# Performance work log

Measured on AMD Instinct MI355X. Metric: run time of the kernel, lower is better.

The kernel has to match this reference:

```python
import jax, jax.numpy as jnp
import numpy as np

N, INC, MID, K = 65536, 256, 64, 16
EPS = 1e-5  # BatchNorm1d default eps


def _bn(x, g, b, m, v):
    # eval-mode BatchNorm1d applied per-channel along the last dim
    return (x - m) * (g * jax.lax.rsqrt(v + EPS)) + b


def setup_inputs() -> dict:
    key = jax.random.key(0)
    ks = jax.random.split(key, 40)
    rn = lambda i, shape, s=0.05: (jax.random.normal(ks[i], shape, jnp.float32) * s)
    pv = lambda i, n: jax.random.uniform(ks[i], (n,), jnp.float32, 0.5, 1.5)  # positive running var
    return {
        "feats": jax.random.normal(ks[0], (N, INC), jnp.float32),
        "pos": jax.random.uniform(ks[1], (N, 3), jnp.float32) * 10.0,
        "idx": jax.random.randint(ks[2], (N, K), 0, N),
        "w_in": rn(3, (MID, INC)),
        "w_q": rn(4, (MID, MID)), "b_q": rn(5, (MID,)),
        "w_k": rn(6, (MID, MID)), "b_k": rn(7, (MID,)),
        "w_v": rn(8, (MID, MID)), "b_v": rn(9, (MID,)),
        # pos_enc: Linear(3,3) -> BN(3) -> ReLU -> Linear(3,mid) -> BN(mid) -> ReLU
        "pe_w1": rn(10, (3, 3)), "pe_b1": rn(11, (3,)),
        "pe_g1": jnp.ones(3), "pe_be1": rn(12, (3,)), "pe_m1": rn(13, (3,)), "pe_v1": pv(14, 3),
        "pe_w2": rn(15, (MID, 3)), "pe_b2": rn(16, (MID,)),
        "pe_g2": jnp.ones(MID), "pe_be2": rn(17, (MID,)), "pe_m2": rn(18, (MID,)), "pe_v2": pv(19, MID),
        # mlp_gamma: Linear(mid,mid) -> BN(mid) -> ReLU -> Linear(mid,mid) -> BN(mid) -> ReLU
        "ga_w1": rn(20, (MID, MID)), "ga_b1": rn(21, (MID,)),
        "ga_g1": jnp.ones(MID), "ga_be1": rn(22, (MID,)), "ga_m1": rn(23, (MID,)), "ga_v1": pv(24, MID),
        "ga_w2": rn(25, (MID, MID)), "ga_b2": rn(26, (MID,)),
        "ga_g2": jnp.ones(MID), "ga_be2": rn(27, (MID,)), "ga_m2": rn(28, (MID,)), "ga_v2": pv(29, MID),
        "w_out": rn(30, (INC, MID)),
    }


def reference(feats, pos, w_in, w_q, b_q, w_k, b_k, w_v, b_v,
              pe_w1, pe_b1, pe_g1, pe_be1, pe_m1, pe_v1,
              pe_w2, pe_b2, pe_g2, pe_be2, pe_m2, pe_v2,
              ga_w1, ga_b1, ga_g1, ga_be1, ga_m1, ga_v1,
              ga_w2, ga_b2, ga_g2, ga_be2, ga_m2, ga_v2,
              w_out, idx):
    xx = feats @ w_in.T                              # [N, mid]
    q = xx @ w_q.T + b_q
    k = xx @ w_k.T + b_k
    v = xx @ w_v.T + b_v
    xv = v[idx]                                      # [N, K, mid] gather
    xk = k[idx]                                      # [N, K, mid]
    xpos = pos[idx]                                  # [N, K, 3]
    # pos_enc
    p = jax.nn.relu(_bn(xpos @ pe_w1.T + pe_b1, pe_g1, pe_be1, pe_m1, pe_v1))
    p = jax.nn.relu(_bn(p @ pe_w2.T + pe_b2, pe_g2, pe_be2, pe_m2, pe_v2))  # [N, K, mid]
    # vector attention logits
    w = xk - q[:, None, :] + p                       # [N, K, mid]
    # mlp_gamma
    w = jax.nn.relu(_bn(w @ ga_w1.T + ga_b1, ga_g1, ga_be1, ga_m1, ga_v1))
    w = jax.nn.relu(_bn(w @ ga_w2.T + ga_b2, ga_g2, ga_be2, ga_m2, ga_v2))
    w = jax.nn.softmax(w, axis=1)                    # softmax over neighbors
    out = jnp.sum((xv + p) * w, axis=1)              # [N, mid]
    out = out @ w_out.T                              # [N, inc]
    return out + feats
```

## Files before the change

kernel.cpp:

```cpp
#include <hip/hip_runtime.h>

#define NPTS 65536
#define INC  256
#define MID  64
#define KNB  16
#define WSTR 72

#define WIN_S   0
#define WQ_S    16384
#define WK_S    20480
#define WV_S    24576
#define GA1_S   28672
#define GA2_S   32768
#define WOUT_S  36864
#define NFRAG_ENT 6656

typedef __attribute__((ext_vector_type(8))) short short8;
typedef __attribute__((ext_vector_type(4))) float f32x4;

#define MFMA(a, b, c) __builtin_amdgcn_mfma_f32_16x16x32_bf16((a), (b), (c), 0, 0, 0)
#define WBAR() __builtin_amdgcn_wave_barrier()

__device__ inline float bf2f(unsigned short s) {
    unsigned int u = ((unsigned int)s) << 16;
    return __builtin_bit_cast(float, u);
}
__device__ inline unsigned int pk_bf16(float lo, float hi) {
    unsigned int r;
    asm("v_cvt_pk_bf16_f32 %0, %1, %2" : "=v"(r) : "v"(lo), "v"(hi));
    return r;
}
__device__ inline short f2bf(float f) { return (short)pk_bf16(f, f); }

__device__ inline short8 cvtf8(f32x4 a, f32x4 b) {
    union { unsigned int u[4]; short8 s; } r;
    r.u[0] = pk_bf16(a[0], a[1]); r.u[1] = pk_bf16(a[2], a[3]);
    r.u[2] = pk_bf16(b[0], b[1]); r.u[3] = pk_bf16(b[2], b[3]);
    return r.s;
}
__device__ inline short8 load_cvt8(const float* __restrict__ p) {
    const f32x4* v = (const f32x4*)p;
    return cvtf8(v[0], v[1]);
}
__device__ inline short8 load_cvt8s(const float* __restrict__ p, float scale) {
    const f32x4* v = (const f32x4*)p;
    f32x4 a = v[0], b = v[1];
    #pragma unroll
    for (int i = 0; i < 4; i++) { a[i] *= scale; b[i] *= scale; }
    return cvtf8(a, b);
}

__global__ __launch_bounds__(256) void k_prep(
    const float* __restrict__ w_in, const float* __restrict__ w_q,
    const float* __restrict__ w_k, const float* __restrict__ w_v,
    const float* __restrict__ ga_w1, const float* __restrict__ ga_w2,
    const float* __restrict__ w_out,
    const float* __restrict__ ga_g1, const float* __restrict__ ga_v1,
    const float* __restrict__ ga_g2, const float* __restrict__ ga_v2,
    short* __restrict__ wbuf)
{
    int gid = blockIdx.x * 256 + threadIdx.x;
    if (gid >= NFRAG_ENT) return;
    if (gid < 2048) {
        int e = gid, f = e >> 6, ln = e & 63;
        int nt = f & 3, ks = f >> 2;
        int row = nt * 16 + (ln & 15), col = ks * 32 + (ln >> 4) * 8;
        *(short8*)&wbuf[(size_t)gid * 8] = load_cvt8(w_in + (size_t)row * INC + col);
    } else if (gid < 4608) {
        int seg = (gid - 2048) >> 9;
        int e = (gid - 2048) & 511;
        const float* m = seg == 0 ? w_q : seg == 1 ? w_k : seg == 2 ? w_v
                       : seg == 3 ? ga_w1 : ga_w2;
        int f = e >> 6, ln = e & 63;
        int nt = f & 3, ks = f >> 2;
        int row = nt * 16 + (ln & 15), col = ks * 32 + (ln >> 4) * 8;
        float scale = 1.f;
        if (seg == 3)      scale = ga_g1[row] * rsqrtf(ga_v1[row] + 1e-5f);
        else if (seg == 4) scale = ga_g2[row] * rsqrtf(ga_v2[row] + 1e-5f);
        *(short8*)&wbuf[(size_t)gid * 8] = load_cvt8s(m + (size_t)row * MID + col, scale);
    } else {
        int e = gid - 4608, f = e >> 6, ln = e & 63;
        int nt = f >> 1, ks = f & 1;
        int row = nt * 16 + (ln & 15), col = ks * 32 + (ln >> 4) * 8;
        *(short8*)&wbuf[(size_t)gid * 8] = load_cvt8(w_out + (size_t)row * MID + col);
    }
}

__global__ __launch_bounds__(256) void k_qkv(
    const float* __restrict__ feats, const short* __restrict__ wfrag,
    const float* __restrict__ pos,
    const float* __restrict__ b_q, const float* __restrict__ b_k,
    const float* __restrict__ b_v,
    const float* __restrict__ pe_w1, const float* __restrict__ pe_b1,
    const float* __restrict__ pe_g1, const float* __restrict__ pe_be1,
    const float* __restrict__ pe_m1, const float* __restrict__ pe_v1,
    const float* __restrict__ pe_w2, const float* __restrict__ pe_b2,
    const float* __restrict__ pe_g2, const float* __restrict__ pe_be2,
    const float* __restrict__ pe_m2, const float* __restrict__ pe_v2,
    const float* __restrict__ ga_b1, const float* __restrict__ ga_g1,
    const float* __restrict__ ga_be1, const float* __restrict__ ga_m1,
    const float* __restrict__ ga_v1,
    short* __restrict__ q1f_out, unsigned* __restrict__ kv_out)
{
    __shared__ __align__(16) short XL[4][16 * WSTR];
    __shared__ float PS[4][16 * 4];
    const int tid = threadIdx.x;
    const int wave = tid >> 6, lane = tid & 63;
    const int l15 = lane & 15, quad = lane >> 4;
    const int rb = (blockIdx.x * 4 + wave) * 16;

    if (lane < 16) {
        float s0 = pe_g1[0] * rsqrtf(pe_v1[0] + 1e-5f);
        float s1 = pe_g1[1] * rsqrtf(pe_v1[1] + 1e-5f);
        float sc = pe_g1[2] * rsqrtf(pe_v1[2] + 1e-5f);
        float px = pos[(size_t)(rb + lane) * 3 + 0];
        float py = pos[(size_t)(rb + lane) * 3 + 1];
        float pz = pos[(size_t)(rb + lane) * 3 + 2];
        PS[wave][lane * 4 + 0] =
            fmaxf((px * pe_w1[0] + py * pe_w1[1] + pz * pe_w1[2] + pe_b1[0] - pe_m1[0]) * s0 + pe_be1[0], 0.f);
        PS[wave][lane * 4 + 1] =
            fmaxf((px * pe_w1[3] + py * pe_w1[4] + pz * pe_w1[5] + pe_b1[1] - pe_m1[1]) * s1 + pe_be1[1], 0.f);
        PS[wave][lane * 4 + 2] =
            fmaxf((px * pe_w1[6] + py * pe_w1[7] + pz * pe_w1[8] + pe_b1[2] - pe_m1[2]) * sc + pe_be1[2], 0.f);
    }

    float w2c0[4], w2c1[4], w2c2[4], s2c[4], sh2c[4], bet1[4], bqc[4], bkc[4], bvc[4];
    #pragma unroll
    for (int nt = 0; nt < 4; nt++) {
        int ch = nt * 16 + l15;
        w2c0[nt] = pe_w2[ch * 3 + 0]; w2c1[nt] = pe_w2[ch * 3 + 1]; w2c2[nt] = pe_w2[ch * 3 + 2];
        float s2 = pe_g2[ch] * rsqrtf(pe_v2[ch] + 1e-5f);
        s2c[nt] = s2;
        sh2c[nt] = (pe_b2[ch] - pe_m2[ch]) * s2 + pe_be2[ch];
        float s1 = ga_g1[ch] * rsqrtf(ga_v1[ch] + 1e-5f);
        bet1[nt] = ga_b1[ch] * s1 + ga_be1[ch] - ga_m1[ch] * s1;
        bqc[nt] = b_q[ch]; bkc[nt] = b_k[ch]; bvc[nt] = b_v[ch];
    }

    f32x4 acc[4];
    #pragma unroll
    for (int nt = 0; nt < 4; nt++) acc[nt] = (f32x4){0.f, 0.f, 0.f, 0.f};
    const float* arow = feats + (size_t)(rb + l15) * INC + quad * 8;
    #pragma unroll
    for (int ks = 0; ks < 8; ks++) {
        short8 a = load_cvt8(arow + ks * 32);
        #pragma unroll
        for (int nt = 0; nt < 4; nt++) {
            short8 b = *(const short8*)&wfrag[WIN_S + (size_t)((ks * 4 + nt) * 64 + lane) * 8];
            acc[nt] = MFMA(a, b, acc[nt]);
        }
    }
    #pragma unroll
    for (int nt = 0; nt < 4; nt++) {
        unsigned int p01 = pk_bf16(acc[nt][0], acc[nt][1]);
        unsigned int p23 = pk_bf16(acc[nt][2], acc[nt][3]);
        XL[wave][(quad * 4 + 0) * WSTR + nt * 16 + l15] = (short)p01;
        XL[wave][(quad * 4 + 1) * WSTR + nt * 16 + l15] = (short)(p01 >> 16);
        XL[wave][(quad * 4 + 2) * WSTR + nt * 16 + l15] = (short)p23;
        XL[wave][(quad * 4 + 3) * WSTR + nt * 16 + l15] = (short)(p23 >> 16);
    }
    WBAR();
    short8 a0 = *(const short8*)&XL[wave][l15 * WSTR + quad * 8];
    short8 a1 = *(const short8*)&XL[wave][l15 * WSTR + 32 + quad * 8];
    WBAR();

    float p10[4], p11[4], p12[4];
    #pragma unroll
    for (int r = 0; r < 4; r++) {
        p10[r] = PS[wave][(quad * 4 + r) * 4 + 0];
        p11[r] = PS[wave][(quad * 4 + r) * 4 + 1];
        p12[r] = PS[wave][(quad * 4 + r) * 4 + 2];
    }
    float pe_[4][4];
    #pragma unroll
    for (int nt = 0; nt < 4; nt++)
        #pragma unroll
        for (int r = 0; r < 4; r++)
            pe_[nt][r] = fmaxf((p10[r] * w2c0[nt] + p11[r] * w2c1[nt] + p12[r] * w2c2[nt])
                               * s2c[nt] + sh2c[nt], 0.f);

    #pragma unroll
    for (int nt = 0; nt < 4; nt++) {
        short8 b0 = *(const short8*)&wfrag[WQ_S + (size_t)((nt) * 64 + lane) * 8];
        short8 b1 = *(const short8*)&wfrag[WQ_S + (size_t)((4 + nt) * 64 + lane) * 8];
        f32x4 c = (f32x4){0.f, 0.f, 0.f, 0.f};
        c = MFMA(a0, b0, c); c = MFMA(a1, b1, c);
        unsigned int p01 = pk_bf16(c[0] + bqc[nt], c[1] + bqc[nt]);
        unsigned int p23 = pk_bf16(c[2] + bqc[nt], c[3] + bqc[nt]);
        XL[wave][(quad * 4 + 0) * WSTR + nt * 16 + l15] = (short)p01;
        XL[wave][(quad * 4 + 1) * WSTR + nt * 16 + l15] = (short)(p01 >> 16);
        XL[wave][(quad * 4 + 2) * WSTR + nt * 16 + l15] = (short)p23;
        XL[wave][(quad * 4 + 3) * WSTR + nt * 16 + l15] = (short)(p23 >> 16);
    }
    WBAR();
    short8 aq0 = *(const short8*)&XL[wave][l15 * WSTR + quad * 8];
    short8 aq1 = *(const short8*)&XL[wave][l15 * WSTR + 32 + quad * 8];
    WBAR();
    #pragma unroll
    for (int nt = 0; nt < 4; nt++) {
        short8 b0 = *(const short8*)&wfrag[GA1_S + (size_t)((nt) * 64 + lane) * 8];
        short8 b1 = *(const short8*)&wfrag[GA1_S + (size_t)((4 + nt) * 64 + lane) * 8];
        f32x4 c = (f32x4){0.f, 0.f, 0.f, 0.f};
        c = MFMA(aq0, b0, c); c = MFMA(aq1, b1, c);
        unsigned int p01 = pk_bf16(c[0] - bet1[nt], c[1] - bet1[nt]);
        unsigned int p23 = pk_bf16(c[2] - bet1[nt], c[3] - bet1[nt]);
        q1f_out[(unsigned)(rb + quad * 4 + 0) * 64u + nt * 16 + l15] = (short)p01;
        q1f_out[(unsigned)(rb + quad * 4 + 1) * 64u + nt * 16 + l15] = (short)(p01 >> 16);
        q1f_out[(unsigned)(rb + quad * 4 + 2) * 64u + nt * 16 + l15] = (short)p23;
        q1f_out[(unsigned)(rb + quad * 4 + 3) * 64u + nt * 16 + l15] = (short)(p23 >> 16);
    }

    WBAR();
    #pragma unroll
    for (int nt = 0; nt < 4; nt++) {
        short8 b0 = *(const short8*)&wfrag[WK_S + (size_t)((nt) * 64 + lane) * 8];
        short8 b1 = *(const short8*)&wfrag[WK_S + (size_t)((4 + nt) * 64 + lane) * 8];
        f32x4 c = (f32x4){0.f, 0.f, 0.f, 0.f};
        c = MFMA(a0, b0, c); c = MFMA(a1, b1, c);
        unsigned int p01 = pk_bf16(c[0] + bkc[nt] + pe_[nt][0], c[1] + bkc[nt] + pe_[nt][1]);
        unsigned int p23 = pk_bf16(c[2] + bkc[nt] + pe_[nt][2], c[3] + bkc[nt] + pe_[nt][3]);
        XL[wave][(quad * 4 + 0) * WSTR + nt * 16 + l15] = (short)p01;
        XL[wave][(quad * 4 + 1) * WSTR + nt * 16 + l15] = (short)(p01 >> 16);
        XL[wave][(quad * 4 + 2) * WSTR + nt * 16 + l15] = (short)p23;
        XL[wave][(quad * 4 + 3) * WSTR + nt * 16 + l15] = (short)(p23 >> 16);
    }
    WBAR();
    short8 ak0 = *(const short8*)&XL[wave][l15 * WSTR + quad * 8];
    short8 ak1 = *(const short8*)&XL[wave][l15 * WSTR + 32 + quad * 8];
    WBAR();
    float k1f[4][4];
    #pragma unroll
    for (int nt = 0; nt < 4; nt++) {
        short8 b0 = *(const short8*)&wfrag[GA1_S + (size_t)((nt) * 64 + lane) * 8];
        short8 b1 = *(const short8*)&wfrag[GA1_S + (size_t)((4 + nt) * 64 + lane) * 8];
        f32x4 c = (f32x4){0.f, 0.f, 0.f, 0.f};
        c = MFMA(ak0, b0, c); c = MFMA(ak1, b1, c);
        #pragma unroll
        for (int r = 0; r < 4; r++) k1f[nt][r] = c[r];
    }

    #pragma unroll
    for (int nt = 0; nt < 4; nt++) {
        short8 b0 = *(const short8*)&wfrag[WV_S + (size_t)((nt) * 64 + lane) * 8];
        short8 b1 = *(const short8*)&wfrag[WV_S + (size_t)((4 + nt) * 64 + lane) * 8];
        f32x4 c = (f32x4){0.f, 0.f, 0.f, 0.f};
        c = MFMA(a0, b0, c); c = MFMA(a1, b1, c);
        #pragma unroll
        for (int r = 0; r < 4; r++) {
            float vv = c[r] + bvc[nt] + pe_[nt][r];
            kv_out[(unsigned)(rb + quad * 4 + r) * 64u + nt * 16 + l15] =
                pk_bf16(k1f[nt][r], vv);
        }
    }
}

#define GATHER(KVN, IT2)                                                      \
    _Pragma("unroll")                                                         \
    for (int j = 0; j < KNB; j++) {                                           \
        int mj = __builtin_amdgcn_readlane(m_all, (IT2) * 16 + j);            \
        KVN[j] = kvbuf[(unsigned)mj * 64u + (unsigned)lane];                  \
    }

#define ATTN_POINT(IT, KV, QV)                                                \
    {                                                                         \
        _Pragma("unroll")                                                     \
        for (int j = 0; j < KNB; j += 2) {                                    \
            float h0 = fmaxf(__builtin_bit_cast(float, KV[j] << 16) - (QV), 0.f);     \
            float h1 = fmaxf(__builtin_bit_cast(float, KV[j + 1] << 16) - (QV), 0.f); \
            unsigned pkw = pk_bf16(h0, h1);                                   \
            Wb[wave][(j) * WSTR + lane] = (short)pkw;                         \
            Wb[wave][(j + 1) * WSTR + lane] = (short)(pkw >> 16);             \
        }                                                                     \
        short8 c0 = *(const short8*)&Wb[wave][l15 * WSTR + quad * 8];         \
        short8 c1 = *(const short8*)&Wb[wave][l15 * WSTR + 32 + quad * 8];    \
        float smv[4][4];                                                      \
        _Pragma("unroll")                                                     \
        for (int nt = 0; nt < 4; nt++) {                                      \
            short8 b0 = *(const short8*)&BW[(size_t)((nt) * 64 + lane) * 8];  \
            short8 b1 = *(const short8*)&BW[(size_t)((4 + nt) * 64 + lane) * 8]; \
            f32x4 c = (f32x4){0.f, 0.f, 0.f, 0.f};                            \
            c = MFMA(c0, b0, c); c = MFMA(c1, b1, c);                         \
            float b2v = B2[nt * 16 + l15];                                    \
            _Pragma("unroll")                                                 \
            for (int r = 0; r < 4; r++)                                       \
                smv[nt][r] = fmaxf(c[r] + b2v, 0.f);                          \
        }                                                                     \
        _Pragma("unroll")                                                     \
        for (int nt = 0; nt < 4; nt++) {                                      \
            float mx = fmaxf(fmaxf(smv[nt][0], smv[nt][1]),                   \
                             fmaxf(smv[nt][2], smv[nt][3]));                  \
            mx = fmaxf(mx, __shfl_xor(mx, 16));                               \
            mx = fmaxf(mx, __shfl_xor(mx, 32));                               \
            float e0 = __expf(smv[nt][0] - mx), e1 = __expf(smv[nt][1] - mx); \
            float e2 = __expf(smv[nt][2] - mx), e3 = __expf(smv[nt][3] - mx); \
            float s = e0 + e1 + e2 + e3;                                      \
            s += __shfl_xor(s, 16);                                           \
            s += __shfl_xor(s, 32);                                           \
            float inv = 1.0f / s;                                             \
            unsigned p01 = pk_bf16(e0 * inv, e1 * inv);                       \
            unsigned p23 = pk_bf16(e2 * inv, e3 * inv);                       \
            Wb[wave][(quad * 4 + 0) * WSTR + nt * 16 + l15] = (short)p01;     \
            Wb[wave][(quad * 4 + 1) * WSTR + nt * 16 + l15] = (short)(p01 >> 16); \
            Wb[wave][(quad * 4 + 2) * WSTR + nt * 16 + l15] = (short)p23;     \
            Wb[wave][(quad * 4 + 3) * WSTR + nt * 16 + l15] = (short)(p23 >> 16); \
        }                                                                     \
        float oacc = 0.f;                                                     \
        _Pragma("unroll")                                                     \
        for (int j = 0; j < KNB; j++)                                         \
            oacc += __builtin_bit_cast(float, KV[j] & 0xffff0000u)            \
                    * bf2f((unsigned short)Wb[wave][j * WSTR + lane]);        \
        OM[((IT) * 4 + wave) * WSTR + lane] = f2bf(oacc);                     \
    }

__global__ __launch_bounds__(256) void k_attn(
    const int* __restrict__ idx,
    const unsigned short* __restrict__ q1f,
    const unsigned* __restrict__ kvbuf, const short* __restrict__ wfrag,
    const float* __restrict__ ga_b2, const float* __restrict__ ga_g2,
    const float* __restrict__ ga_be2, const float* __restrict__ ga_m2,
    const float* __restrict__ ga_v2,
    const float* __restrict__ feats, float* __restrict__ out)
{
    __shared__ __align__(16) short BW[512 * 8];
    __shared__ __align__(16) short Wb[4][16 * WSTR];
    __shared__ __align__(16) short OM[16 * WSTR];
    __shared__ float B2[64];

    const int tid = threadIdx.x;
    const int wave = tid >> 6, lane = tid & 63;
    const int l15 = lane & 15, quad = lane >> 4;

    #pragma unroll
    for (int rep = 0; rep < 2; rep++) {
        int e = rep * 256 + tid;
        *(short8*)&BW[(size_t)e * 8] = *(const short8*)&wfrag[GA2_S + (size_t)e * 8];
    }
    if (tid < 64) {
        float s2 = ga_g2[tid] * rsqrtf(ga_v2[tid] + 1e-5f);
        B2[tid] = ga_b2[tid] * s2 + ga_be2[tid] - ga_m2[tid] * s2;
    }
    __syncthreads();

    const int n0 = blockIdx.x * 16 + wave;
    int m_all = idx[(unsigned)(n0 + (lane >> 4) * 4) * 16u + (unsigned)(lane & 15)];
    float qf0 = bf2f(q1f[(unsigned)(n0     ) * 64u + lane]);
    float qf1 = bf2f(q1f[(unsigned)(n0 +  4) * 64u + lane]);
    float qf2 = bf2f(q1f[(unsigned)(n0 +  8) * 64u + lane]);
    float qf3 = bf2f(q1f[(unsigned)(n0 + 12) * 64u + lane]);

    unsigned kvA[KNB], kvB[KNB];
    GATHER(kvA, 0)
    GATHER(kvB, 1)
    ATTN_POINT(0, kvA, qf0)
    GATHER(kvA, 2)
    ATTN_POINT(1, kvB, qf1)
    GATHER(kvB, 3)
    ATTN_POINT(2, kvA, qf2)
    ATTN_POINT(3, kvB, qf3)

    __syncthreads();
    short8 A0 = *(const short8*)&OM[l15 * WSTR + quad * 8];
    short8 A1 = *(const short8*)&OM[l15 * WSTR + 32 + quad * 8];
    const int rb = blockIdx.x * 16;
    #pragma unroll
    for (int t = 0; t < 4; t++) {
        int nt = wave * 4 + t;
        short8 b0 = *(const short8*)&wfrag[WOUT_S + (size_t)((nt * 2 + 0) * 64 + lane) * 8];
        short8 b1 = *(const short8*)&wfrag[WOUT_S + (size_t)((nt * 2 + 1) * 64 + lane) * 8];
        f32x4 c = (f32x4){0.f, 0.f, 0.f, 0.f};
        c = MFMA(A0, b0, c);
        c = MFMA(A1, b1, c);
        #pragma unroll
        for (int r = 0; r < 4; r++) {
            size_t off = (size_t)(rb + quad * 4 + r) * INC + nt * 16 + l15;
            out[off] = c[r] + feats[off];
        }
    }
}

extern "C" void kernel_launch(void* const* d_in, const int* in_sizes, int n_in,
                              void* d_out, int out_size, void* d_ws, size_t ws_size,
                              hipStream_t stream)
{
    const float* feats = (const float*)d_in[0];
    const float* pos   = (const float*)d_in[1];
    const int*   idx   = (const int*)d_in[2];
    const float* w_in  = (const float*)d_in[3];
    const float* w_q   = (const float*)d_in[4];
    const float* b_q   = (const float*)d_in[5];
    const float* w_k   = (const float*)d_in[6];
    const float* b_k   = (const float*)d_in[7];
    const float* w_v   = (const float*)d_in[8];
    const float* b_v   = (const float*)d_in[9];
    const float* pe_w1 = (const float*)d_in[10];
    const float* pe_b1 = (const float*)d_in[11];
    const float* pe_g1 = (const float*)d_in[12];
    const float* pe_be1= (const float*)d_in[13];
    const float* pe_m1 = (const float*)d_in[14];
    const float* pe_v1 = (const float*)d_in[15];
    const float* pe_w2 = (const float*)d_in[16];
    const float* pe_b2 = (const float*)d_in[17];
    const float* pe_g2 = (const float*)d_in[18];
    const float* pe_be2= (const float*)d_in[19];
    const float* pe_m2 = (const float*)d_in[20];
    const float* pe_v2 = (const float*)d_in[21];
    const float* ga_w1 = (const float*)d_in[22];
    const float* ga_b1 = (const float*)d_in[23];
    const float* ga_g1 = (const float*)d_in[24];
    const float* ga_be1= (const float*)d_in[25];
    const float* ga_m1 = (const float*)d_in[26];
    const float* ga_v1 = (const float*)d_in[27];
    const float* ga_w2 = (const float*)d_in[28];
    const float* ga_b2 = (const float*)d_in[29];
    const float* ga_g2 = (const float*)d_in[30];
    const float* ga_be2= (const float*)d_in[31];
    const float* ga_m2 = (const float*)d_in[32];
    const float* ga_v2 = (const float*)d_in[33];
    const float* w_out = (const float*)d_in[34];

    char* ws = (char*)d_ws;
    short*    q1f  = (short*)(ws);
    unsigned* kv   = (unsigned*)(ws + (size_t) 8 * 1024 * 1024);
    short*    wbuf = (short*)(ws + (size_t)24 * 1024 * 1024);

    k_prep<<<26, 256, 0, stream>>>(w_in, w_q, w_k, w_v, ga_w1, ga_w2, w_out,
                                   ga_g1, ga_v1, ga_g2, ga_v2, wbuf);
    k_qkv<<<NPTS / 64, 256, 0, stream>>>(feats, wbuf, pos, b_q, b_k, b_v,
                                         pe_w1, pe_b1, pe_g1, pe_be1, pe_m1, pe_v1,
                                         pe_w2, pe_b2, pe_g2, pe_be2, pe_m2, pe_v2,
                                         ga_b1, ga_g1, ga_be1, ga_m1, ga_v1,
                                         q1f, kv);
    k_attn<<<NPTS / 16, 256, 0, stream>>>(idx,
                                          (const unsigned short*)q1f, kv, wbuf,
                                          ga_b2, ga_g2, ga_be2, ga_m2, ga_v2,
                                          feats, (float*)d_out);
}
```

Before: 254.3 us.

## Fold q and gamma-layer-1 weights, drop softmax max, double-buffer attention LDS

The prep kernel now precomputes the product of the BN-scaled ga_w1 and w_q, plus a fused bias, so the qkv kernel does one 64x64 MFMA stage for the q-projection path instead of two and skips an LDS round trip. In the attention kernel the softmax drops the max-subtraction shuffles and defers the division to the final weighted sum. It also gives each wave two LDS scratch buffers, alternating between neighbouring points to reduce write-after-read hazards. Skipping the max is only safe because the logits are ReLU outputs, but large logits could still overflow exp. Folding the two matrices in fp32 before bf16 rounding slightly changes the rounding.

```diff
diff --git a/kernel.cpp b/kernel.cpp
--- a/kernel.cpp
+++ b/kernel.cpp
@@ -14,6 +14,7 @@
 #define GA2_S   32768
 #define WOUT_S  36864
 #define NFRAG_ENT 6656
+#define BQ1F_S  53248
 
 typedef __attribute__((ext_vector_type(8))) short short8;
 typedef __attribute__((ext_vector_type(4))) float f32x4;
@@ -54,13 +55,15 @@
     const float* __restrict__ w_in, const float* __restrict__ w_q,
     const float* __restrict__ w_k, const float* __restrict__ w_v,
     const float* __restrict__ ga_w1, const float* __restrict__ ga_w2,
-    const float* __restrict__ w_out,
+    const float* __restrict__ w_out, const float* __restrict__ b_q,
     const float* __restrict__ ga_g1, const float* __restrict__ ga_v1,
+    const float* __restrict__ ga_b1, const float* __restrict__ ga_be1,
+    const float* __restrict__ ga_m1,
     const float* __restrict__ ga_g2, const float* __restrict__ ga_v2,
     short* __restrict__ wbuf)
 {
     int gid = blockIdx.x * 256 + threadIdx.x;
-    if (gid >= NFRAG_ENT) return;
+    if (gid >= NFRAG_ENT + 64) return;
     if (gid < 2048) {
         int e = gid, f = e >> 6, ln = e & 63;
         int nt = f & 3, ks = f >> 2;
@@ -69,37 +72,56 @@
     } else if (gid < 4608) {
         int seg = (gid - 2048) >> 9;
         int e = (gid - 2048) & 511;
-        const float* m = seg == 0 ? w_q : seg == 1 ? w_k : seg == 2 ? w_v
-                       : seg == 3 ? ga_w1 : ga_w2;
         int f = e >> 6, ln = e & 63;
         int nt = f & 3, ks = f >> 2;
         int row = nt * 16 + (ln & 15), col = ks * 32 + (ln >> 4) * 8;
-        float scale = 1.f;
-        if (seg == 3)      scale = ga_g1[row] * rsqrtf(ga_v1[row] + 1e-5f);
-        else if (seg == 4) scale = ga_g2[row] * rsqrtf(ga_v2[row] + 1e-5f);
-        *(short8*)&wbuf[(size_t)gid * 8] = load_cvt8s(m + (size_t)row * MID + col, scale);
-    } else {
+        if (seg == 0) {
+            float s1r = ga_g1[row] * rsqrtf(ga_v1[row] + 1e-5f);
+            float accv[8];
+            #pragma unroll
+            for (int o = 0; o < 8; o++) accv[o] = 0.f;
+            for (int c = 0; c < 64; c++) {
+                float a = ga_w1[(size_t)row * MID + c] * s1r;
+                #pragma unroll
+                for (int o = 0; o < 8; o++)
+                    accv[o] += a * w_q[(size_t)c * MID + col + o];
+            }
+            f32x4 lo = {accv[0], accv[1], accv[2], accv[3]};
+            f32x4 hi = {accv[4], accv[5], accv[6], accv[7]};
+            *(short8*)&wbuf[(size_t)gid * 8] = cvtf8(lo, hi);
+        } else {
+            const float* m = seg == 1 ? w_k : seg == 2 ? w_v
+                           : seg == 3 ? ga_w1 : ga_w2;
+            float scale = 1.f;
+            if (seg == 3)      scale = ga_g1[row] * rsqrtf(ga_v1[row] + 1e-5f);
+            else if (seg == 4) scale = ga_g2[row] * rsqrtf(ga_v2[row] + 1e-5f);
+            *(short8*)&wbuf[(size_t)gid * 8] = load_cvt8s(m + (size_t)row * MID + col, scale);
+        }
+    } else if (gid < NFRAG_ENT) {
         int e = gid - 4608, f = e >> 6, ln = e & 63;
         int nt = f >> 1, ks = f & 1;
         int row = nt * 16 + (ln & 15), col = ks * 32 + (ln >> 4) * 8;
         *(short8*)&wbuf[(size_t)gid * 8] = load_cvt8(w_out + (size_t)row * MID + col);
+    } else {
+        int ch = gid - NFRAG_ENT;
+        float s1r = ga_g1[ch] * rsqrtf(ga_v1[ch] + 1e-5f);
+        float acc = 0.f;
+        for (int c = 0; c < 64; c++) acc += ga_w1[(size_t)ch * MID + c] * b_q[c];
+        float beta1 = (ga_b1[ch] - ga_m1[ch]) * s1r + ga_be1[ch];
+        ((float*)(wbuf + BQ1F_S))[ch] = s1r * acc - beta1;
     }
 }
 
 __global__ __launch_bounds__(256) void k_qkv(
     const float* __restrict__ feats, const short* __restrict__ wfrag,
     const float* __restrict__ pos,
-    const float* __restrict__ b_q, const float* __restrict__ b_k,
-    const float* __restrict__ b_v,
+    const float* __restrict__ b_k, const float* __restrict__ b_v,
     const float* __restrict__ pe_w1, const float* __restrict__ pe_b1,
     const float* __restrict__ pe_g1, const float* __restrict__ pe_be1,
     const float* __restrict__ pe_m1, const float* __restrict__ pe_v1,
     const float* __restrict__ pe_w2, const float* __restrict__ pe_b2,
     const float* __restrict__ pe_g2, const float* __restrict__ pe_be2,
     const float* __restrict__ pe_m2, const float* __restrict__ pe_v2,
-    const float* __restrict__ ga_b1, const float* __restrict__ ga_g1,
-    const float* __restrict__ ga_be1, const float* __restrict__ ga_m1,
-    const float* __restrict__ ga_v1,
     short* __restrict__ q1f_out, unsigned* __restrict__ kv_out)
 {
     __shared__ __align__(16) short XL[4][16 * WSTR];
@@ -124,7 +146,8 @@
             fmaxf((px * pe_w1[6] + py * pe_w1[7] + pz * pe_w1[8] + pe_b1[2] - pe_m1[2]) * sc + pe_be1[2], 0.f);
     }
 
-    float w2c0[4], w2c1[4], w2c2[4], s2c[4], sh2c[4], bet1[4], bqc[4], bkc[4], bvc[4];
+    const float* bq1f = (const float*)(wfrag + BQ1F_S);
+    float w2c0[4], w2c1[4], w2c2[4], s2c[4], sh2c[4], bq1c[4], bkc[4], bvc[4];
     #pragma unroll
     for (int nt = 0; nt < 4; nt++) {
         int ch = nt * 16 + l15;
@@ -132,9 +155,8 @@
         float s2 = pe_g2[ch] * rsqrtf(pe_v2[ch] + 1e-5f);
         s2c[nt] = s2;
         sh2c[nt] = (pe_b2[ch] - pe_m2[ch]) * s2 + pe_be2[ch];
-        float s1 = ga_g1[ch] * rsqrtf(ga_v1[ch] + 1e-5f);
-        bet1[nt] = ga_b1[ch] * s1 + ga_be1[ch] - ga_m1[ch] * s1;
-        bqc[nt] = b_q[ch]; bkc[nt] = b_k[ch]; bvc[nt] = b_v[ch];
+        bq1c[nt] = bq1f[ch];
+        bkc[nt] = b_k[ch]; bvc[nt] = b_v[ch];
     }
 
     f32x4 acc[4];
@@ -185,25 +207,8 @@
         short8 b1 = *(const short8*)&wfrag[WQ_S + (size_t)((4 + nt) * 64 + lane) * 8];
         f32x4 c = (f32x4){0.f, 0.f, 0.f, 0.f};
         c = MFMA(a0, b0, c); c = MFMA(a1, b1, c);
-        unsigned int p01 = pk_bf16(c[0] + bqc[nt], c[1] + bqc[nt]);
-        unsigned int p23 = pk_bf16(c[2] + bqc[nt], c[3] + bqc[nt]);
-        XL[wave][(quad * 4 + 0) * WSTR + nt * 16 + l15] = (short)p01;
-        XL[wave][(quad * 4 + 1) * WSTR + nt * 16 + l15] = (short)(p01 >> 16);
-        XL[wave][(quad * 4 + 2) * WSTR + nt * 16 + l15] = (short)p23;
-        XL[wave][(quad * 4 + 3) * WSTR + nt * 16 + l15] = (short)(p23 >> 16);
-    }
-    WBAR();
-    short8 aq0 = *(const short8*)&XL[wave][l15 * WSTR + quad * 8];
-    short8 aq1 = *(const short8*)&XL[wave][l15 * WSTR + 32 + quad * 8];
-    WBAR();
-    #pragma unroll
-    for (int nt = 0; nt < 4; nt++) {
-        short8 b0 = *(const short8*)&wfrag[GA1_S + (size_t)((nt) * 64 + lane) * 8];
-        short8 b1 = *(const short8*)&wfrag[GA1_S + (size_t)((4 + nt) * 64 + lane) * 8];
-        f32x4 c = (f32x4){0.f, 0.f, 0.f, 0.f};
-        c = MFMA(aq0, b0, c); c = MFMA(aq1, b1, c);
-        unsigned int p01 = pk_bf16(c[0] - bet1[nt], c[1] - bet1[nt]);
-        unsigned int p23 = pk_bf16(c[2] - bet1[nt], c[3] - bet1[nt]);
+        unsigned int p01 = pk_bf16(c[0] + bq1c[nt], c[1] + bq1c[nt]);
+        unsigned int p23 = pk_bf16(c[2] + bq1c[nt], c[3] + bq1c[nt]);
         q1f_out[(unsigned)(rb + quad * 4 + 0) * 64u + nt * 16 + l15] = (short)p01;
         q1f_out[(unsigned)(rb + quad * 4 + 1) * 64u + nt * 16 + l15] = (short)(p01 >> 16);
         q1f_out[(unsigned)(rb + quad * 4 + 2) * 64u + nt * 16 + l15] = (short)p23;
@@ -261,18 +266,19 @@
         KVN[j] = kvbuf[(unsigned)mj * 64u + (unsigned)lane];                  \
     }
 
-#define ATTN_POINT(IT, KV, QV)                                                \
+#define ATTN_POINT(IT, KV, QV, WB)                                            \
     {                                                                         \
+        short* wb_ = (WB);                                                    \
         _Pragma("unroll")                                                     \
         for (int j = 0; j < KNB; j += 2) {                                    \
             float h0 = fmaxf(__builtin_bit_cast(float, KV[j] << 16) - (QV), 0.f);     \
             float h1 = fmaxf(__builtin_bit_cast(float, KV[j + 1] << 16) - (QV), 0.f); \
             unsigned pkw = pk_bf16(h0, h1);                                   \
-            Wb[wave][(j) * WSTR + lane] = (short)pkw;                         \
-            Wb[wave][(j + 1) * WSTR + lane] = (short)(pkw >> 16);             \
+            wb_[(j) * WSTR + lane] = (short)pkw;                              \
+            wb_[(j + 1) * WSTR + lane] = (short)(pkw >> 16);                  \
         }                                                                     \
-        short8 c0 = *(const short8*)&Wb[wave][l15 * WSTR + quad * 8];         \
-        short8 c1 = *(const short8*)&Wb[wave][l15 * WSTR + 32 + quad * 8];    \
+        short8 c0 = *(const short8*)&wb_[l15 * WSTR + quad * 8];              \
+        short8 c1 = *(const short8*)&wb_[l15 * WSTR + 32 + quad * 8];         \
         float smv[4][4];                                                      \
         _Pragma("unroll")                                                     \
         for (int nt = 0; nt < 4; nt++) {                                      \
@@ -285,31 +291,31 @@
             for (int r = 0; r < 4; r++)                                       \
                 smv[nt][r] = fmaxf(c[r] + b2v, 0.f);                          \
         }                                                                     \
+        float sarr[4];                                                        \
         _Pragma("unroll")                                                     \
         for (int nt = 0; nt < 4; nt++) {                                      \
-            float mx = fmaxf(fmaxf(smv[nt][0], smv[nt][1]),                   \
-                             fmaxf(smv[nt][2], smv[nt][3]));                  \
-            mx = fmaxf(mx, __shfl_xor(mx, 16));                               \
-            mx = fmaxf(mx, __shfl_xor(mx, 32));                               \
-            float e0 = __expf(smv[nt][0] - mx), e1 = __expf(smv[nt][1] - mx); \
-            float e2 = __expf(smv[nt][2] - mx), e3 = __expf(smv[nt][3] - mx); \
+            float e0 = __expf(smv[nt][0]), e1 = __expf(smv[nt][1]);           \
+            float e2 = __expf(smv[nt][2]), e3 = __expf(smv[nt][3]);           \
             float s = e0 + e1 + e2 + e3;                                      \
             s += __shfl_xor(s, 16);                                           \
             s += __shfl_xor(s, 32);                                           \
-            float inv = 1.0f / s;                                             \
-            unsigned p01 = pk_bf16(e0 * inv, e1 * inv);                       \
-            unsigned p23 = pk_bf16(e2 * inv, e3 * inv);                       \
-            Wb[wave][(quad * 4 + 0) * WSTR + nt * 16 + l15] = (short)p01;     \
-            Wb[wave][(quad * 4 + 1) * WSTR + nt * 16 + l15] = (short)(p01 >> 16); \
-            Wb[wave][(quad * 4 + 2) * WSTR + nt * 16 + l15] = (short)p23;     \
-            Wb[wave][(quad * 4 + 3) * WSTR + nt * 16 + l15] = (short)(p23 >> 16); \
+            sarr[nt] = s;                                                     \
+            unsigned p01 = pk_bf16(e0, e1);                                   \
+            unsigned p23 = pk_bf16(e2, e3);                                   \
+            wb_[(quad * 4 + 0) * WSTR + nt * 16 + l15] = (short)p01;          \
+            wb_[(quad * 4 + 1) * WSTR + nt * 16 + l15] = (short)(p01 >> 16);  \
+            wb_[(quad * 4 + 2) * WSTR + nt * 16 + l15] = (short)p23;          \
+            wb_[(quad * 4 + 3) * WSTR + nt * 16 + l15] = (short)(p23 >> 16);  \
         }                                                                     \
         float oacc = 0.f;                                                     \
         _Pragma("unroll")                                                     \
         for (int j = 0; j < KNB; j++)                                         \
             oacc += __builtin_bit_cast(float, KV[j] & 0xffff0000u)            \
-                    * bf2f((unsigned short)Wb[wave][j * WSTR + lane]);        \
-        OM[((IT) * 4 + wave) * WSTR + lane] = f2bf(oacc);                     \
+                    * bf2f((unsigned short)wb_[j * WSTR + lane]);             \
+        float s01 = (quad == 0) ? sarr[0] : sarr[1];                          \
+        float s23 = (quad == 2) ? sarr[2] : sarr[3];                          \
+        float ssel = (quad < 2) ? s01 : s23;                                  \
+        OM[((IT) * 4 + wave) * WSTR + lane] = f2bf(oacc * (1.0f / ssel));     \
     }
 
 __global__ __launch_bounds__(256) void k_attn(
@@ -322,7 +328,7 @@
     const float* __restrict__ feats, float* __restrict__ out)
 {
     __shared__ __align__(16) short BW[512 * 8];
-    __shared__ __align__(16) short Wb[4][16 * WSTR];
+    __shared__ __align__(16) short Wb[4][2][16 * WSTR];
     __shared__ __align__(16) short OM[16 * WSTR];
     __shared__ float B2[64];
 
@@ -351,12 +357,12 @@
     unsigned kvA[KNB], kvB[KNB];
     GATHER(kvA, 0)
     GATHER(kvB, 1)
-    ATTN_POINT(0, kvA, qf0)
+    ATTN_POINT(0, kvA, qf0, &Wb[wave][0][0])
     GATHER(kvA, 2)
-    ATTN_POINT(1, kvB, qf1)
+    ATTN_POINT(1, kvB, qf1, &Wb[wave][1][0])
     GATHER(kvB, 3)
-    ATTN_POINT(2, kvA, qf2)
-    ATTN_POINT(3, kvB, qf3)
+    ATTN_POINT(2, kvA, qf2, &Wb[wave][0][0])
+    ATTN_POINT(3, kvB, qf3, &Wb[wave][1][0])
 
     __syncthreads();
     short8 A0 = *(const short8*)&OM[l15 * WSTR + quad * 8];
@@ -423,12 +429,12 @@
     unsigned* kv   = (unsigned*)(ws + (size_t) 8 * 1024 * 1024);
     short*    wbuf = (short*)(ws + (size_t)24 * 1024 * 1024);
 
-    k_prep<<<26, 256, 0, stream>>>(w_in, w_q, w_k, w_v, ga_w1, ga_w2, w_out,
-                                   ga_g1, ga_v1, ga_g2, ga_v2, wbuf);
-    k_qkv<<<NPTS / 64, 256, 0, stream>>>(feats, wbuf, pos, b_q, b_k, b_v,
+    k_prep<<<27, 256, 0, stream>>>(w_in, w_q, w_k, w_v, ga_w1, ga_w2, w_out, b_q,
+                                   ga_g1, ga_v1, ga_b1, ga_be1, ga_m1,
+                                   ga_g2, ga_v2, wbuf);
+    k_qkv<<<NPTS / 64, 256, 0, stream>>>(feats, wbuf, pos, b_k, b_v,
                                          pe_w1, pe_b1, pe_g1, pe_be1, pe_m1, pe_v1,
                                          pe_w2, pe_b2, pe_g2, pe_be2, pe_m2, pe_v2,
-                                         ga_b1, ga_g1, ga_be1, ga_m1, ga_v1,
                                          q1f, kv);
     k_attn<<<NPTS / 16, 256, 0, stream>>>(idx,
                                           (const unsigned short*)q1f, kv, wbuf,
```

After: 249.4 us. No clear change (-1.9%).
